# Optimization experiments

Hardware: AMD Instinct MI355X
Metric: run time of the kernel (lower is better)

Reference implementation:

```python
import jax, jax.numpy as jnp
import numpy as np

B, N, D, H = 64, 257, 1024, 16
HD = D // H  # 64


def setup_inputs() -> dict:
    key = jax.random.key(0)
    k1, k2, k3, k4, k5, k6 = jax.random.split(key, 6)
    x = jax.random.normal(k1, (B, N, D), dtype=jnp.float32)
    # boolean key mask per batch; never mask CLS token (col 0) so no fully-masked rows
    mask = jax.random.randint(k2, (B, N), 0, 2) > 0
    mask = mask.at[:, 0].set(False)
    s = 1.0 / np.sqrt(D)
    in_proj_w = jax.random.normal(k3, (3 * D, D), dtype=jnp.float32) * s
    in_proj_b = jax.random.normal(k4, (3 * D,), dtype=jnp.float32) * 0.02
    out_proj_w = jax.random.normal(k5, (D, D), dtype=jnp.float32) * s
    out_proj_b = jax.random.normal(k6, (D,), dtype=jnp.float32) * 0.02
    return {"x": x, "mask": mask, "in_proj_w": in_proj_w, "in_proj_b": in_proj_b,
            "out_proj_w": out_proj_w, "out_proj_b": out_proj_b}


def reference(x, mask, in_proj_w, in_proj_b, out_proj_w, out_proj_b):
    b, n, d = x.shape
    h, hd = H, d // H
    # fused QKV projection: [b, n, 3*d]
    qkv = jnp.einsum('bnd,ed->bne', x, in_proj_w) + in_proj_b
    # einops 'b n (qkv h d) -> qkv b h n d'
    qkv = qkv.reshape(b, n, 3, h, hd).transpose(2, 0, 3, 1, 4)
    q, k, v = qkv[0], qkv[1], qkv[2]  # each [b, h, n, hd]
    attn_weights = jnp.einsum('bhqe,bhke->bhqk', q, k) / jnp.sqrt(jnp.asarray(hd, x.dtype))
    # mode == 'mask': -inf on masked keys (broadcast over heads and queries)
    attn_weights = jnp.where(mask[:, None, None, :], -jnp.inf, attn_weights)
    attn_matrix = jax.nn.softmax(attn_weights, axis=-1)
    out = jnp.einsum('bhqk,bhke->bhqe', attn_matrix, v)  # [b, h, n, hd]
    out = out.transpose(0, 2, 1, 3).reshape(b, n, d)      # 'b h n d -> b n (h d)'
    return jnp.einsum('bnd,ed->bne', out, out_proj_w) + out_proj_b
```

## Files before the change

### kernel.cpp

```cpp
#include <hip/hip_runtime.h>

#define B_   64
#define N_   257
#define D_   1024
#define H_   16
#define HD_  64
#define M_   (B_*N_)
#define MPAD 16512
#define CK_  96
#define PLS_ 104

typedef __bf16 bf16x8 __attribute__((ext_vector_type(8)));
typedef __bf16 bf16x4 __attribute__((ext_vector_type(4)));
typedef float  f32x4  __attribute__((ext_vector_type(4)));

__device__ __forceinline__ void gload_lds16(const void* g, void* l) {
    __builtin_amdgcn_global_load_lds(
        (const __attribute__((address_space(1))) void*)g,
        (__attribute__((address_space(3))) void*)l, 16, 0, 0);
}

__device__ __forceinline__ int vswz(int cg, int hd) {
    int s = (hd >> 3) & 7;
    return cg < 8 ? (cg ^ s) : (8 + ((cg & 3) ^ (s & 3)));
}

__global__ __launch_bounds__(256) void cvt_f32_bf16(const float* __restrict__ src,
                                                    __bf16* __restrict__ dst, int n4) {
    int i = blockIdx.x * 256 + threadIdx.x;
    if (i >= n4) return;
    float4 v = reinterpret_cast<const float4*>(src)[i];
    bf16x4 o;
    o[0] = (__bf16)v.x; o[1] = (__bf16)v.y; o[2] = (__bf16)v.z; o[3] = (__bf16)v.w;
    *reinterpret_cast<bf16x4*>(dst + (size_t)i * 4) = o;
}

__global__ __launch_bounds__(256) void qkv_gemm(const __bf16* __restrict__ A,
                                                const __bf16* __restrict__ W,
                                                const float* __restrict__ bias,
                                                __bf16* __restrict__ qw,
                                                __bf16* __restrict__ kw,
                                                __bf16* __restrict__ vw) {
    __shared__ __align__(16) __bf16 As[128 * 32];
    __shared__ __align__(16) __bf16 Ws[128 * 32];
    const int tid  = threadIdx.x;
    const int row0 = blockIdx.x * 128, col0 = blockIdx.y * 128;
    const int lane = tid & 63, wv = tid >> 6;
    const int wm = (wv >> 1) * 64, wn = (wv & 1) * 64;
    const int fr = lane & 15, fq = lane >> 4;
    const int c1 = tid + 256;
    const size_t ga0 = (size_t)(row0 + (tid >> 2)) * 1024 + (tid & 3) * 8;
    const size_t ga1 = (size_t)(row0 + (c1 >> 2)) * 1024 + (c1 & 3) * 8;
    const size_t gw0 = (size_t)(col0 + (tid >> 2)) * 1024 + (tid & 3) * 8;
    const size_t gw1 = (size_t)(col0 + (c1 >> 2)) * 1024 + (c1 & 3) * 8;
    char* lbase0 = (char*)As + wv * 1024;
    char* lbase1 = (char*)As + wv * 1024 + 4096;
    char* lbw0 = (char*)Ws + wv * 1024;
    char* lbw1 = (char*)Ws + wv * 1024 + 4096;
    f32x4 acc[4][4] = {};
    for (int k0 = 0; k0 < 1024; k0 += 32) {
        gload_lds16(A + ga0 + k0, lbase0);
        gload_lds16(A + ga1 + k0, lbase1);
        gload_lds16(W + gw0 + k0, lbw0);
        gload_lds16(W + gw1 + k0, lbw1);
        __syncthreads();
        bf16x8 af[4], bfr[4];
#pragma unroll
        for (int i = 0; i < 4; ++i)
            af[i] = *reinterpret_cast<const bf16x8*>(&As[(wm + i * 16 + fr) * 32 + fq * 8]);
#pragma unroll
        for (int j = 0; j < 4; ++j)
            bfr[j] = *reinterpret_cast<const bf16x8*>(&Ws[(wn + j * 16 + fr) * 32 + fq * 8]);
#pragma unroll
        for (int i = 0; i < 4; ++i)
#pragma unroll
            for (int j = 0; j < 4; ++j)
                acc[i][j] = __builtin_amdgcn_mfma_f32_16x16x32_bf16(af[i], bfr[j], acc[i][j], 0, 0, 0);
        __syncthreads();
    }
    const int which = col0 >> 10;
    __bf16* dst = which == 0 ? qw : (which == 1 ? kw : vw);
    const float scale = which == 0 ? 0.125f : 1.0f;
    float bj[4];
#pragma unroll
    for (int j = 0; j < 4; ++j) bj[j] = bias[col0 + wn + j * 16 + fr];
    const int h = ((col0 + wn + fr) >> 6) & 15;
    const int hdb = fr;
#pragma unroll
    for (int i = 0; i < 4; ++i) {
#pragma unroll
        for (int r = 0; r < 4; ++r) {
            const int m = row0 + wm + i * 16 + fq * 4 + r;
            if (m < M_) {
                const int bb = m / 257, nn = m % 257;
                __bf16* p = dst + ((size_t)(bb * 16 + h) * 257 + nn) * 64 + hdb;
#pragma unroll
                for (int j = 0; j < 4; ++j)
                    p[j * 16] = (__bf16)((acc[i][j][r] + bj[j]) * scale);
            }
        }
    }
}

__global__ __launch_bounds__(256) void attn_kernel(const __bf16* __restrict__ qw,
                                                   const __bf16* __restrict__ kw,
                                                   const __bf16* __restrict__ vw,
                                                   const int* __restrict__ mask,
                                                   __bf16* __restrict__ attn) {
    const int bh = blockIdx.x;
    const int bb = bh >> 4, hh = bh & 15;
    const int q0 = blockIdx.y * 64;
    const int tid = threadIdx.x, lane = tid & 63, wv = tid >> 6;
    const int fr = lane & 15, fq = lane >> 4;
    const float NEG_INF = -__builtin_inff();

    __shared__ __align__(16) __bf16 Qs[64 * 64];
    __shared__ __align__(16) __bf16 Ks[CK_ * 64];
    __shared__ __align__(16) __bf16 Vt[64 * CK_];
    __shared__ __align__(16) __bf16 Pl[4][16 * PLS_];
    __shared__ float maskb[CK_];

    const __bf16* qg = qw + ((size_t)bh * 257 + q0) * 64;
    const __bf16* kg = kw + (size_t)bh * 257 * 64;
    const __bf16* vg = vw + (size_t)bh * 257 * 64;
    const int* mg = mask + bb * 257;

    {
        if (q0 + (tid >> 3) < 257)
            gload_lds16(qg + (size_t)(tid >> 3) * 64 + (tid & 7) * 8, (char*)Qs + wv * 1024);
        const int c = tid + 256;
        if (q0 + (c >> 3) < 257)
            gload_lds16(qg + (size_t)(c >> 3) * 64 + (c & 7) * 8, (char*)Qs + wv * 1024 + 4096);
    }

    float m_run[4] = {NEG_INF, NEG_INF, NEG_INF, NEG_INF};
    float l_run[4] = {};
    f32x4 Oa[4] = {};

    for (int c3 = 0; c3 < 3; ++c3) {
        const int k0 = c3 * CK_;
        __syncthreads();
#pragma unroll
        for (int i = 0; i < 3; ++i) {
            const int c = tid + i * 256;
            if (k0 + (c >> 3) < 257)
                gload_lds16(kg + (size_t)(k0 + (c >> 3)) * 64 + (c & 7) * 8,
                            (char*)Ks + wv * 1024 + i * 4096);
        }
#pragma unroll
        for (int it = 0; it < 3; ++it) {
            const int t = tid + it * 256;
            const int key = t >> 3, grp = t & 7;
            if (k0 + key < 257) {
                bf16x8 v8 = *reinterpret_cast<const bf16x8*>(vg + (size_t)(k0 + key) * 64 + grp * 8);
#pragma unroll
                for (int u = 0; u < 8; ++u) {
                    const int hd = grp * 8 + u;
                    Vt[hd * CK_ + vswz(key >> 3, hd) * 8 + (key & 7)] = v8[u];
                }
            }
        }
        if (tid < CK_) {
            const int j = k0 + tid;
            maskb[tid] = (j < 257 && mg[j] == 0) ? 0.0f : NEG_INF;
        }
        __syncthreads();

        bf16x8 aq[2];
#pragma unroll
        for (int ks = 0; ks < 2; ++ks)
            aq[ks] = *reinterpret_cast<const bf16x8*>(&Qs[(wv * 16 + fr) * 64 + ks * 32 + fq * 8]);
        f32x4 s[6];
#pragma unroll
        for (int nt = 0; nt < 6; ++nt) {
            f32x4 sa = {};
#pragma unroll
            for (int ks = 0; ks < 2; ++ks) {
                bf16x8 bk = *reinterpret_cast<const bf16x8*>(&Ks[(nt * 16 + fr) * 64 + ks * 32 + fq * 8]);
                sa = __builtin_amdgcn_mfma_f32_16x16x32_bf16(aq[ks], bk, sa, 0, 0, 0);
            }
            const float mb = maskb[nt * 16 + fr];
#pragma unroll
            for (int r = 0; r < 4; ++r) sa[r] += mb;
            s[nt] = sa;
        }
        float alpha[4];
#pragma unroll
        for (int r = 0; r < 4; ++r) {
            float v = s[0][r];
#pragma unroll
            for (int nt = 1; nt < 6; ++nt) v = fmaxf(v, s[nt][r]);
            v = fmaxf(v, __shfl_xor(v, 1));
            v = fmaxf(v, __shfl_xor(v, 2));
            v = fmaxf(v, __shfl_xor(v, 4));
            v = fmaxf(v, __shfl_xor(v, 8));
            const float mnew = fmaxf(m_run[r], v);
            alpha[r] = __expf(m_run[r] - mnew);
            m_run[r] = mnew;
        }
        float sm[4] = {};
#pragma unroll
        for (int nt = 0; nt < 6; ++nt)
#pragma unroll
            for (int r = 0; r < 4; ++r) {
                const float p = __expf(s[nt][r] - m_run[r]);
                s[nt][r] = p;
                sm[r] += p;
            }
#pragma unroll
        for (int r = 0; r < 4; ++r) {
            float v = sm[r];
            v += __shfl_xor(v, 1);
            v += __shfl_xor(v, 2);
            v += __shfl_xor(v, 4);
            v += __shfl_xor(v, 8);
            l_run[r] = l_run[r] * alpha[r] + v;
        }
#pragma unroll
        for (int ot = 0; ot < 4; ++ot)
#pragma unroll
            for (int r = 0; r < 4; ++r) Oa[ot][r] *= alpha[r];
#pragma unroll
        for (int nt = 0; nt < 6; ++nt)
#pragma unroll
            for (int r = 0; r < 4; ++r)
                Pl[wv][(fq * 4 + r) * PLS_ + nt * 16 + fr] = (__bf16)s[nt][r];
        __syncthreads();
        bf16x8 ap[3];
#pragma unroll
        for (int kk = 0; kk < 3; ++kk)
            ap[kk] = *reinterpret_cast<const bf16x8*>(&Pl[wv][fr * PLS_ + kk * 32 + fq * 8]);
#pragma unroll
        for (int ot = 0; ot < 4; ++ot) {
            const int row = ot * 16 + fr;
#pragma unroll
            for (int kk = 0; kk < 3; ++kk) {
                bf16x8 bv = *reinterpret_cast<const bf16x8*>(&Vt[row * CK_ + vswz(kk * 4 + fq, row) * 8]);
                Oa[ot] = __builtin_amdgcn_mfma_f32_16x16x32_bf16(ap[kk], bv, Oa[ot], 0, 0, 0);
            }
        }
    }
#pragma unroll
    for (int r = 0; r < 4; ++r) {
        const int n = q0 + wv * 16 + fq * 4 + r;
        if (n < 257) {
            const float inv = 1.0f / l_run[r];
#pragma unroll
            for (int ot = 0; ot < 4; ++ot)
                attn[((size_t)(bb * 257 + n)) * 1024 + hh * 64 + ot * 16 + fr] =
                    (__bf16)(Oa[ot][r] * inv);
        }
    }
}

__global__ __launch_bounds__(256) void out_gemm(const __bf16* __restrict__ A,
                                                const __bf16* __restrict__ W,
                                                const float* __restrict__ bias,
                                                float* __restrict__ out) {
    __shared__ __align__(16) __bf16 As[128 * 32];
    __shared__ __align__(16) __bf16 Ws[128 * 32];
    const int tid  = threadIdx.x;
    const int row0 = blockIdx.x * 128, col0 = blockIdx.y * 128;
    const int lane = tid & 63, wv = tid >> 6;
    const int wm = (wv >> 1) * 64, wn = (wv & 1) * 64;
    const int fr = lane & 15, fq = lane >> 4;
    const int c1 = tid + 256;
    const size_t ga0 = (size_t)(row0 + (tid >> 2)) * 1024 + (tid & 3) * 8;
    const size_t ga1 = (size_t)(row0 + (c1 >> 2)) * 1024 + (c1 & 3) * 8;
    const size_t gw0 = (size_t)(col0 + (tid >> 2)) * 1024 + (tid & 3) * 8;
    const size_t gw1 = (size_t)(col0 + (c1 >> 2)) * 1024 + (c1 & 3) * 8;
    char* lbase0 = (char*)As + wv * 1024;
    char* lbase1 = (char*)As + wv * 1024 + 4096;
    char* lbw0 = (char*)Ws + wv * 1024;
    char* lbw1 = (char*)Ws + wv * 1024 + 4096;
    f32x4 acc[4][4] = {};
    for (int k0 = 0; k0 < 1024; k0 += 32) {
        gload_lds16(A + ga0 + k0, lbase0);
        gload_lds16(A + ga1 + k0, lbase1);
        gload_lds16(W + gw0 + k0, lbw0);
        gload_lds16(W + gw1 + k0, lbw1);
        __syncthreads();
        bf16x8 af[4], bfr[4];
#pragma unroll
        for (int i = 0; i < 4; ++i)
            af[i] = *reinterpret_cast<const bf16x8*>(&As[(wm + i * 16 + fr) * 32 + fq * 8]);
#pragma unroll
        for (int j = 0; j < 4; ++j)
            bfr[j] = *reinterpret_cast<const bf16x8*>(&Ws[(wn + j * 16 + fr) * 32 + fq * 8]);
#pragma unroll
        for (int i = 0; i < 4; ++i)
#pragma unroll
            for (int j = 0; j < 4; ++j)
                acc[i][j] = __builtin_amdgcn_mfma_f32_16x16x32_bf16(af[i], bfr[j], acc[i][j], 0, 0, 0);
        __syncthreads();
    }
    float bj[4];
#pragma unroll
    for (int j = 0; j < 4; ++j) bj[j] = bias[col0 + wn + j * 16 + fr];
#pragma unroll
    for (int i = 0; i < 4; ++i)
#pragma unroll
        for (int r = 0; r < 4; ++r) {
            const int m = row0 + wm + i * 16 + fq * 4 + r;
            if (m < M_) {
                float* p = out + (size_t)m * 1024 + col0 + wn + fr;
#pragma unroll
                for (int j = 0; j < 4; ++j) p[j * 16] = acc[i][j][r] + bj[j];
            }
        }
}

extern "C" void kernel_launch(void* const* d_in, const int* in_sizes, int n_in,
                              void* d_out, int out_size, void* d_ws, size_t ws_size,
                              hipStream_t stream) {
    const float* x  = (const float*)d_in[0];
    const int* mask = (const int*)d_in[1];
    const float* w1 = (const float*)d_in[2];
    const float* b1 = (const float*)d_in[3];
    const float* w2 = (const float*)d_in[4];
    const float* b2 = (const float*)d_in[5];
    float* out = (float*)d_out;
    char* ws = (char*)d_ws;
    __bf16* x_bf  = (__bf16*)(ws);
    __bf16* w1_bf = (__bf16*)(ws + 33816576);
    __bf16* w2_bf = (__bf16*)(ws + 40108032);
    __bf16* q_ws  = (__bf16*)(ws + 42205184);
    __bf16* k_ws  = (__bf16*)(ws + 75890688);
    __bf16* v_ws  = (__bf16*)(ws + 109576192);
    __bf16* a_bf  = (__bf16*)(ws + 143261696);

    cvt_f32_bf16<<<16448, 256, 0, stream>>>(x, x_bf, 4210688);
    cvt_f32_bf16<<<3072, 256, 0, stream>>>(w1, w1_bf, 786432);
    cvt_f32_bf16<<<1024, 256, 0, stream>>>(w2, w2_bf, 262144);
    qkv_gemm<<<dim3(129, 24), 256, 0, stream>>>(x_bf, w1_bf, b1, q_ws, k_ws, v_ws);
    attn_kernel<<<dim3(1024, 5), 256, 0, stream>>>(q_ws, k_ws, v_ws, mask, a_bf);
    out_gemm<<<dim3(129, 8), 256, 0, stream>>>(a_bf, w2_bf, b2, out);
}
```

Measured before the change: 469.1 us.

## Swizzle LDS tiles, widen GEMM K-step, stage QKV stores through LDS

Both GEMMs now load 64-wide K tiles with an XOR swizzle on the 16-byte groups, which halves the barrier count per K loop and aims to remove LDS bank conflicts on the MFMA fragment reads. The QKV epilogue writes the output tile to LDS first, then does 16-byte coalesced stores into the per-head Q/K/V layout instead of scattered 2-byte writes. The attention kernel uses the same XOR swizzle for Q, K and a padded V-transpose, and precomputes the full mask once instead of per chunk. In exchange, LDS use per GEMM block doubles to 32KB, which may lower occupancy.

```diff
diff --git a/kernel.cpp b/kernel.cpp
--- a/kernel.cpp
+++ b/kernel.cpp
@@ -6,8 +6,8 @@
 #define H_   16
 #define HD_  64
 #define M_   (B_*N_)
-#define MPAD 16512
 #define CK_  96
+#define VTS_ 128
 #define PLS_ 104
 
 typedef __bf16 bf16x8 __attribute__((ext_vector_type(8)));
@@ -18,11 +18,6 @@
     __builtin_amdgcn_global_load_lds(
         (const __attribute__((address_space(1))) void*)g,
         (__attribute__((address_space(3))) void*)l, 16, 0, 0);
-}
-
-__device__ __forceinline__ int vswz(int cg, int hd) {
-    int s = (hd >> 3) & 7;
-    return cg < 8 ? (cg ^ s) : (8 + ((cg & 3) ^ (s & 3)));
 }
 
 __global__ __launch_bounds__(256) void cvt_f32_bf16(const float* __restrict__ src,
@@ -41,41 +36,48 @@
                                                 __bf16* __restrict__ qw,
                                                 __bf16* __restrict__ kw,
                                                 __bf16* __restrict__ vw) {
-    __shared__ __align__(16) __bf16 As[128 * 32];
-    __shared__ __align__(16) __bf16 Ws[128 * 32];
+    __shared__ __align__(16) char smem[32768];
+    __bf16* As = (__bf16*)smem;
+    __bf16* Ws = (__bf16*)(smem + 16384);
+    __bf16* Ct = (__bf16*)smem;
     const int tid  = threadIdx.x;
     const int row0 = blockIdx.x * 128, col0 = blockIdx.y * 128;
     const int lane = tid & 63, wv = tid >> 6;
     const int wm = (wv >> 1) * 64, wn = (wv & 1) * 64;
     const int fr = lane & 15, fq = lane >> 4;
-    const int c1 = tid + 256;
-    const size_t ga0 = (size_t)(row0 + (tid >> 2)) * 1024 + (tid & 3) * 8;
-    const size_t ga1 = (size_t)(row0 + (c1 >> 2)) * 1024 + (c1 & 3) * 8;
-    const size_t gw0 = (size_t)(col0 + (tid >> 2)) * 1024 + (tid & 3) * 8;
-    const size_t gw1 = (size_t)(col0 + (c1 >> 2)) * 1024 + (c1 & 3) * 8;
-    char* lbase0 = (char*)As + wv * 1024;
-    char* lbase1 = (char*)As + wv * 1024 + 4096;
-    char* lbw0 = (char*)Ws + wv * 1024;
-    char* lbw1 = (char*)Ws + wv * 1024 + 4096;
+    size_t sA[4], sW[4];
+#pragma unroll
+    for (int i = 0; i < 4; ++i) {
+        const int c = tid + i * 256;
+        const int r = c >> 3, g = (c & 7) ^ (r & 7);
+        sA[i] = (size_t)(row0 + r) * 1024 + g * 8;
+        sW[i] = (size_t)(col0 + r) * 1024 + g * 8;
+    }
+    const int fsw = ((fr & 7)) * 8;
     f32x4 acc[4][4] = {};
-    for (int k0 = 0; k0 < 1024; k0 += 32) {
-        gload_lds16(A + ga0 + k0, lbase0);
-        gload_lds16(A + ga1 + k0, lbase1);
-        gload_lds16(W + gw0 + k0, lbw0);
-        gload_lds16(W + gw1 + k0, lbw1);
-        __syncthreads();
-        bf16x8 af[4], bfr[4];
-#pragma unroll
-        for (int i = 0; i < 4; ++i)
-            af[i] = *reinterpret_cast<const bf16x8*>(&As[(wm + i * 16 + fr) * 32 + fq * 8]);
-#pragma unroll
-        for (int j = 0; j < 4; ++j)
-            bfr[j] = *reinterpret_cast<const bf16x8*>(&Ws[(wn + j * 16 + fr) * 32 + fq * 8]);
-#pragma unroll
-        for (int i = 0; i < 4; ++i)
+    for (int k0 = 0; k0 < 1024; k0 += 64) {
+#pragma unroll
+        for (int i = 0; i < 4; ++i) {
+            gload_lds16(A + sA[i] + k0, (char*)As + i * 4096 + wv * 1024);
+            gload_lds16(W + sW[i] + k0, (char*)Ws + i * 4096 + wv * 1024);
+        }
+        __syncthreads();
+#pragma unroll
+        for (int ks = 0; ks < 2; ++ks) {
+            const int goff = (((ks * 4 + fq) ^ (fr & 7)) * 8);
+            bf16x8 af[4], bw[4];
+#pragma unroll
+            for (int i = 0; i < 4; ++i)
+                af[i] = *reinterpret_cast<const bf16x8*>(&As[(wm + i * 16 + fr) * 64 + goff]);
 #pragma unroll
             for (int j = 0; j < 4; ++j)
-                acc[i][j] = __builtin_amdgcn_mfma_f32_16x16x32_bf16(af[i], bfr[j], acc[i][j], 0, 0, 0);
+                bw[j] = *reinterpret_cast<const bf16x8*>(&Ws[(wn + j * 16 + fr) * 64 + goff]);
+#pragma unroll
+            for (int i = 0; i < 4; ++i)
+#pragma unroll
+                for (int j = 0; j < 4; ++j)
+                    acc[i][j] = __builtin_amdgcn_mfma_f32_16x16x32_bf16(af[i], bw[j], acc[i][j], 0, 0, 0);
+        }
         __syncthreads();
     }
     const int which = col0 >> 10;
@@ -84,20 +86,27 @@
     float bj[4];
 #pragma unroll
     for (int j = 0; j < 4; ++j) bj[j] = bias[col0 + wn + j * 16 + fr];
-    const int h = ((col0 + wn + fr) >> 6) & 15;
-    const int hdb = fr;
-#pragma unroll
-    for (int i = 0; i < 4; ++i) {
+#pragma unroll
+    for (int i = 0; i < 4; ++i)
 #pragma unroll
         for (int r = 0; r < 4; ++r) {
-            const int m = row0 + wm + i * 16 + fq * 4 + r;
-            if (m < M_) {
-                const int bb = m / 257, nn = m % 257;
-                __bf16* p = dst + ((size_t)(bb * 16 + h) * 257 + nn) * 64 + hdb;
-#pragma unroll
-                for (int j = 0; j < 4; ++j)
-                    p[j * 16] = (__bf16)((acc[i][j][r] + bj[j]) * scale);
-            }
+            const int row = wm + i * 16 + fq * 4 + r;
+#pragma unroll
+            for (int j = 0; j < 4; ++j)
+                Ct[row * 128 + wn + j * 16 + fr] = (__bf16)((acc[i][j][r] + bj[j]) * scale);
+        }
+    __syncthreads();
+    const int h0 = (col0 >> 6) & 15;
+    const int col = (tid & 15) * 8;
+    const int h = h0 + (col >> 6), hd = col & 63;
+#pragma unroll
+    for (int p = 0; p < 8; ++p) {
+        const int row = p * 16 + (tid >> 4);
+        const int m = row0 + row;
+        if (m < M_) {
+            bf16x8 v = *reinterpret_cast<const bf16x8*>(&Ct[row * 128 + col]);
+            const int bb = m / 257, nn = m - bb * 257;
+            *reinterpret_cast<bf16x8*>(dst + ((size_t)(bb * 16 + h) * 257 + nn) * 64 + hd) = v;
         }
     }
 }
@@ -116,21 +125,24 @@
 
     __shared__ __align__(16) __bf16 Qs[64 * 64];
     __shared__ __align__(16) __bf16 Ks[CK_ * 64];
-    __shared__ __align__(16) __bf16 Vt[64 * CK_];
+    __shared__ __align__(16) __bf16 Vt[64 * VTS_];
     __shared__ __align__(16) __bf16 Pl[4][16 * PLS_];
-    __shared__ float maskb[CK_];
+    __shared__ float maskb[288];
 
     const __bf16* qg = qw + ((size_t)bh * 257 + q0) * 64;
     const __bf16* kg = kw + (size_t)bh * 257 * 64;
     const __bf16* vg = vw + (size_t)bh * 257 * 64;
     const int* mg = mask + bb * 257;
 
-    {
-        if (q0 + (tid >> 3) < 257)
-            gload_lds16(qg + (size_t)(tid >> 3) * 64 + (tid & 7) * 8, (char*)Qs + wv * 1024);
-        const int c = tid + 256;
-        if (q0 + (c >> 3) < 257)
-            gload_lds16(qg + (size_t)(c >> 3) * 64 + (c & 7) * 8, (char*)Qs + wv * 1024 + 4096);
+    for (int idx = tid; idx < 288; idx += 256)
+        maskb[idx] = (idx < 257 && mg[idx] == 0) ? 0.0f : NEG_INF;
+
+#pragma unroll
+    for (int i = 0; i < 2; ++i) {
+        const int c = tid + i * 256;
+        const int r = c >> 3, g = (c & 7) ^ (r & 7);
+        if (q0 + r < 257)
+            gload_lds16(qg + (size_t)r * 64 + g * 8, (char*)Qs + i * 4096 + wv * 1024);
     }
 
     float m_run[4] = {NEG_INF, NEG_INF, NEG_INF, NEG_INF};
@@ -143,9 +155,9 @@
 #pragma unroll
         for (int i = 0; i < 3; ++i) {
             const int c = tid + i * 256;
-            if (k0 + (c >> 3) < 257)
-                gload_lds16(kg + (size_t)(k0 + (c >> 3)) * 64 + (c & 7) * 8,
-                            (char*)Ks + wv * 1024 + i * 4096);
+            const int r = c >> 3, g = (c & 7) ^ (r & 7);
+            if (k0 + r < 257)
+                gload_lds16(kg + (size_t)(k0 + r) * 64 + g * 8, (char*)Ks + i * 4096 + wv * 1024);
         }
 #pragma unroll
         for (int it = 0; it < 3; ++it) {
@@ -156,33 +168,33 @@
 #pragma unroll
                 for (int u = 0; u < 8; ++u) {
                     const int hd = grp * 8 + u;
-                    Vt[hd * CK_ + vswz(key >> 3, hd) * 8 + (key & 7)] = v8[u];
+                    Vt[hd * VTS_ + (((key >> 3) ^ (hd & 7)) * 8) + (key & 7)] = v8[u];
                 }
             }
         }
-        if (tid < CK_) {
-            const int j = k0 + tid;
-            maskb[tid] = (j < 257 && mg[j] == 0) ? 0.0f : NEG_INF;
-        }
-        __syncthreads();
-
-        bf16x8 aq[2];
-#pragma unroll
-        for (int ks = 0; ks < 2; ++ks)
-            aq[ks] = *reinterpret_cast<const bf16x8*>(&Qs[(wv * 16 + fr) * 64 + ks * 32 + fq * 8]);
+        __syncthreads();
+
         f32x4 s[6];
-#pragma unroll
-        for (int nt = 0; nt < 6; ++nt) {
-            f32x4 sa = {};
-#pragma unroll
-            for (int ks = 0; ks < 2; ++ks) {
-                bf16x8 bk = *reinterpret_cast<const bf16x8*>(&Ks[(nt * 16 + fr) * 64 + ks * 32 + fq * 8]);
-                sa = __builtin_amdgcn_mfma_f32_16x16x32_bf16(aq[ks], bk, sa, 0, 0, 0);
-            }
-            const float mb = maskb[nt * 16 + fr];
-#pragma unroll
-            for (int r = 0; r < 4; ++r) sa[r] += mb;
-            s[nt] = sa;
+        {
+            bf16x8 aq[2];
+#pragma unroll
+            for (int ks = 0; ks < 2; ++ks)
+                aq[ks] = *reinterpret_cast<const bf16x8*>(
+                    &Qs[(wv * 16 + fr) * 64 + (((ks * 4 + fq) ^ (fr & 7)) * 8)]);
+#pragma unroll
+            for (int nt = 0; nt < 6; ++nt) {
+                f32x4 sa = {};
+#pragma unroll
+                for (int ks = 0; ks < 2; ++ks) {
+                    bf16x8 bk = *reinterpret_cast<const bf16x8*>(
+                        &Ks[(nt * 16 + fr) * 64 + (((ks * 4 + fq) ^ (fr & 7)) * 8)]);
+                    sa = __builtin_amdgcn_mfma_f32_16x16x32_bf16(aq[ks], bk, sa, 0, 0, 0);
+                }
+                const float mb = maskb[k0 + nt * 16 + fr];
+#pragma unroll
+                for (int r = 0; r < 4; ++r) sa[r] += mb;
+                s[nt] = sa;
+            }
         }
         float alpha[4];
 #pragma unroll
@@ -235,7 +247,8 @@
             const int row = ot * 16 + fr;
 #pragma unroll
             for (int kk = 0; kk < 3; ++kk) {
-                bf16x8 bv = *reinterpret_cast<const bf16x8*>(&Vt[row * CK_ + vswz(kk * 4 + fq, row) * 8]);
+                bf16x8 bv = *reinterpret_cast<const bf16x8*>(
+                    &Vt[row * VTS_ + (((kk * 4 + fq) ^ (fr & 7)) * 8)]);
                 Oa[ot] = __builtin_amdgcn_mfma_f32_16x16x32_bf16(ap[kk], bv, Oa[ot], 0, 0, 0);
             }
         }
@@ -257,41 +270,46 @@
                                                 const __bf16* __restrict__ W,
                                                 const float* __restrict__ bias,
                                                 float* __restrict__ out) {
-    __shared__ __align__(16) __bf16 As[128 * 32];
-    __shared__ __align__(16) __bf16 Ws[128 * 32];
+    __shared__ __align__(16) char smem[32768];
+    __bf16* As = (__bf16*)smem;
+    __bf16* Ws = (__bf16*)(smem + 16384);
     const int tid  = threadIdx.x;
     const int row0 = blockIdx.x * 128, col0 = blockIdx.y * 128;
     const int lane = tid & 63, wv = tid >> 6;
     const int wm = (wv >> 1) * 64, wn = (wv & 1) * 64;
     const int fr = lane & 15, fq = lane >> 4;
-    const int c1 = tid + 256;
-    const size_t ga0 = (size_t)(row0 + (tid >> 2)) * 1024 + (tid & 3) * 8;
-    const size_t ga1 = (size_t)(row0 + (c1 >> 2)) * 1024 + (c1 & 3) * 8;
-    const size_t gw0 = (size_t)(col0 + (tid >> 2)) * 1024 + (tid & 3) * 8;
-    const size_t gw1 = (size_t)(col0 + (c1 >> 2)) * 1024 + (c1 & 3) * 8;
-    char* lbase0 = (char*)As + wv * 1024;
-    char* lbase1 = (char*)As + wv * 1024 + 4096;
-    char* lbw0 = (char*)Ws + wv * 1024;
-    char* lbw1 = (char*)Ws + wv * 1024 + 4096;
+    size_t sA[4], sW[4];
+#pragma unroll
+    for (int i = 0; i < 4; ++i) {
+        const int c = tid + i * 256;
+        const int r = c >> 3, g = (c & 7) ^ (r & 7);
+        sA[i] = (size_t)(row0 + r) * 1024 + g * 8;
+        sW[i] = (size_t)(col0 + r) * 1024 + g * 8;
+    }
     f32x4 acc[4][4] = {};
-    for (int k0 = 0; k0 < 1024; k0 += 32) {
-        gload_lds16(A + ga0 + k0, lbase0);
-        gload_lds16(A + ga1 + k0, lbase1);
-        gload_lds16(W + gw0 + k0, lbw0);
-        gload_lds16(W + gw1 + k0, lbw1);
-        __syncthreads();
-        bf16x8 af[4], bfr[4];
-#pragma unroll
-        for (int i = 0; i < 4; ++i)
-            af[i] = *reinterpret_cast<const bf16x8*>(&As[(wm + i * 16 + fr) * 32 + fq * 8]);
-#pragma unroll
-        for (int j = 0; j < 4; ++j)
-            bfr[j] = *reinterpret_cast<const bf16x8*>(&Ws[(wn + j * 16 + fr) * 32 + fq * 8]);
-#pragma unroll
-        for (int i = 0; i < 4; ++i)
+    for (int k0 = 0; k0 < 1024; k0 += 64) {
+#pragma unroll
+        for (int i = 0; i < 4; ++i) {
+            gload_lds16(A + sA[i] + k0, (char*)As + i * 4096 + wv * 1024);
+            gload_lds16(W + sW[i] + k0, (char*)Ws + i * 4096 + wv * 1024);
+        }
+        __syncthreads();
+#pragma unroll
+        for (int ks = 0; ks < 2; ++ks) {
+            const int goff = (((ks * 4 + fq) ^ (fr & 7)) * 8);
+            bf16x8 af[4], bw[4];
+#pragma unroll
+            for (int i = 0; i < 4; ++i)
+                af[i] = *reinterpret_cast<const bf16x8*>(&As[(wm + i * 16 + fr) * 64 + goff]);
 #pragma unroll
             for (int j = 0; j < 4; ++j)
-                acc[i][j] = __builtin_amdgcn_mfma_f32_16x16x32_bf16(af[i], bfr[j], acc[i][j], 0, 0, 0);
+                bw[j] = *reinterpret_cast<const bf16x8*>(&Ws[(wn + j * 16 + fr) * 64 + goff]);
+#pragma unroll
+            for (int i = 0; i < 4; ++i)
+#pragma unroll
+                for (int j = 0; j < 4; ++j)
+                    acc[i][j] = __builtin_amdgcn_mfma_f32_16x16x32_bf16(af[i], bw[j], acc[i][j], 0, 0, 0);
+        }
         __syncthreads();
     }
     float bj[4];
```

Result: no change. 468.4 us (-0.2%).
